# Kernel optimization log

Measured on AMD Instinct MI355X. Metric: run time of the kernel, lower is better.

## Reference

```python
import jax, jax.numpy as jnp
import numpy as np

B, T, C, HS = 8, 2048, 1024, 64

def setup_inputs() -> dict:
    key = jax.random.key(0)
    ks = jax.random.split(key, 6)
    return {
        "q_vec": jax.random.normal(ks[0], (B, T, C), dtype=jnp.float32),
        "k_vec": jax.random.normal(ks[1], (B, T, C), dtype=jnp.float32),
        "v_vec": jax.random.normal(ks[2], (B, T, C), dtype=jnp.float32),
        "mask": jnp.ones((B, T), dtype=jnp.int32),
        "Wq": jax.random.normal(ks[3], (C, HS), dtype=jnp.float32) * (C ** -0.5),
        "Wk": jax.random.normal(ks[4], (C, HS), dtype=jnp.float32) * (C ** -0.5),
        "Wv": jax.random.normal(ks[5], (C, HS), dtype=jnp.float32) * (C ** -0.5),
    }

def reference(q_vec, k_vec, v_vec, mask, Wq, Wk, Wv):
    # bias-free linear projections: [B,T,C] @ [C,HS] -> [B,T,HS]
    q = jnp.einsum('btc,ch->bth', q_vec, Wq)
    k = jnp.einsum('btc,ch->bth', k_vec, Wk)
    v = jnp.einsum('btc,ch->bth', v_vec, Wv)
    scale = k.shape[-1] ** -0.5
    # full T x T score matrix, as in the original module
    scores = jnp.einsum('bth,bsh->bts', q, k) * scale  # [B,T,T]
    Tq = scores.shape[1]
    # _expand_along_time: expanded[b,i,j] = mask[b,j], then causal tril
    mask_exp = jnp.broadcast_to(mask[:, None, :].astype(jnp.float32), scores.shape)
    tril = jnp.tril(jnp.ones((Tq, Tq), dtype=jnp.float32))
    combined = mask_exp * tril[None, :, :]
    scores = jnp.where(combined == 0, -jnp.inf, scores)
    attn = jax.nn.softmax(scores, axis=-1)
    # dropout p=0.0 (eval) -> identity
    out = jnp.einsum('bts,bsh->bth', attn, v)  # [B,T,HS]
    return out
```

## Files before the change

### kernel.cpp

```cpp
#include <hip/hip_runtime.h>
#include <hip/hip_bf16.h>
#include <cmath>
#include <stdint.h>

#define B_ 8
#define T_ 2048
#define C_ 1024
#define HS_ 64
#define NS 8
#define LP 72

typedef __attribute__((ext_vector_type(8))) short short8;
typedef __attribute__((ext_vector_type(4))) float floatx4;

__device__ inline unsigned short f2bf(float f) {
    union { float f; unsigned u; } v; v.f = f;
    unsigned r = v.u + 0x7FFF + ((v.u >> 16) & 1);
    return (unsigned short)(r >> 16);
}
__device__ inline unsigned pk2bf(float a, float b) {
    union { __hip_bfloat162 h; unsigned u; } v;
    v.h = __float22bfloat162_rn(float2{a, b});
    return v.u;
}
__device__ inline float bf2f(unsigned short u) {
    union { unsigned u; float f; } w; w.u = ((unsigned)u) << 16; return w.f;
}

__global__ __launch_bounds__(256) void prep_wt(const float* __restrict__ Wq,
                                               const float* __restrict__ Wk,
                                               const float* __restrict__ Wv,
                                               unsigned short* __restrict__ wt) {
    int p = blockIdx.x >> 4;
    int chunk = blockIdx.x & 15;
    const float* W = (p == 0) ? Wq : (p == 1) ? Wk : Wv;
    unsigned short* WT = wt + p * (C_ * HS_);
    int base = chunk * 4096;
    for (int i = threadIdx.x; i < 4096; i += 256) {
        int idx = base + i;
        int k = idx >> 6, n = idx & 63;
        WT[n * C_ + k] = f2bf(W[idx]);
    }
}

__global__ __launch_bounds__(256) void proj_kernel(
    const float* __restrict__ qv, const float* __restrict__ kv, const float* __restrict__ vv,
    const unsigned short* __restrict__ wt,
    unsigned short* __restrict__ qb, unsigned short* __restrict__ kb, unsigned short* __restrict__ vb)
{
    const int tid  = threadIdx.x;
    const int wave = tid >> 6, lane = tid & 63, quad = lane >> 4, l16 = lane & 15;
    const int wid  = blockIdx.x * 4 + wave;
    const int p    = wid >> 10;
    const int tile = wid & 1023;

    const float* X = (p == 0) ? qv : (p == 1) ? kv : vv;
    const unsigned short* WT = wt + p * (C_ * HS_);
    unsigned short* Ob = (p == 0) ? qb : (p == 1) ? kb : vb;
    const float oscale = (p == 0) ? 0.125f : 1.0f;

    const float* xp = X + ((long)tile * 16 + l16) * C_ + quad * 8;
    const unsigned short* wp = WT + l16 * C_ + quad * 8;

    floatx4 acc[4] = { {0,0,0,0},{0,0,0,0},{0,0,0,0},{0,0,0,0} };

    floatx4 xa, xb;
    short8 bfr0, bfr1, bfr2, bfr3;
    xa = *(const floatx4*)(xp);
    xb = *(const floatx4*)(xp + 4);
    bfr0 = *(const short8*)(wp + 0 * 16 * C_);
    bfr1 = *(const short8*)(wp + 1 * 16 * C_);
    bfr2 = *(const short8*)(wp + 2 * 16 * C_);
    bfr3 = *(const short8*)(wp + 3 * 16 * C_);

    #pragma unroll 4
    for (int ks = 0; ks < 32; ++ks) {
        floatx4 cx0 = xa, cx1 = xb;
        short8 cb0 = bfr0, cb1 = bfr1, cb2 = bfr2, cb3 = bfr3;
        if (ks + 1 < 32) {
            const int k0 = (ks + 1) * 32;
            xa = *(const floatx4*)(xp + k0);
            xb = *(const floatx4*)(xp + k0 + 4);
            bfr0 = *(const short8*)(wp + 0 * 16 * C_ + k0);
            bfr1 = *(const short8*)(wp + 1 * 16 * C_ + k0);
            bfr2 = *(const short8*)(wp + 2 * 16 * C_ + k0);
            bfr3 = *(const short8*)(wp + 3 * 16 * C_ + k0);
        }
        union { short8 s; unsigned u[4]; } af;
        af.u[0] = pk2bf(cx0[0], cx0[1]);
        af.u[1] = pk2bf(cx0[2], cx0[3]);
        af.u[2] = pk2bf(cx1[0], cx1[1]);
        af.u[3] = pk2bf(cx1[2], cx1[3]);
        acc[0] = __builtin_amdgcn_mfma_f32_16x16x32_bf16(af.s, cb0, acc[0], 0, 0, 0);
        acc[1] = __builtin_amdgcn_mfma_f32_16x16x32_bf16(af.s, cb1, acc[1], 0, 0, 0);
        acc[2] = __builtin_amdgcn_mfma_f32_16x16x32_bf16(af.s, cb2, acc[2], 0, 0, 0);
        acc[3] = __builtin_amdgcn_mfma_f32_16x16x32_bf16(af.s, cb3, acc[3], 0, 0, 0);
    }

    unsigned short* op = Ob + ((long)tile * 16 + quad * 4) * HS_ + l16;
    #pragma unroll
    for (int nt = 0; nt < 4; ++nt)
        #pragma unroll
        for (int r = 0; r < 4; ++r)
            op[r * HS_ + nt * 16] = f2bf(acc[nt][r] * oscale);
}

__global__ __launch_bounds__(256) void attn_partial(
    const unsigned short* __restrict__ qb, const unsigned short* __restrict__ kb,
    const unsigned short* __restrict__ vb, const int* __restrict__ mask,
    unsigned short* __restrict__ Opart, float* __restrict__ Mpart, float* __restrict__ Lpart)
{
    const int s  = blockIdx.x & (NS - 1);
    const int bq = blockIdx.x >> 3;
    const int qt = bq & 31;
    const int b  = bq >> 5;
    if (s > qt) return;

    __shared__ unsigned short Klds[64 * LP];
    __shared__ unsigned short Vt[64 * LP];
    __shared__ unsigned short Plds[4][16 * LP];

    const int tid = threadIdx.x;
    const int wave = tid >> 6, lane = tid & 63, quad = lane >> 4, l16 = lane & 15;

    const int qrow = qt * 64 + wave * 16 + l16;
    const unsigned short* qp = qb + ((long)(b * T_ + qrow)) * HS_;
    short8 aq0 = *(const short8*)&qp[0  + quad * 8];
    short8 aq1 = *(const short8*)&qp[32 + quad * 8];

    floatx4 acc_o[4] = { {0,0,0,0},{0,0,0,0},{0,0,0,0},{0,0,0,0} };
    float m_r[4] = { -INFINITY, -INFINITY, -INFINITY, -INFINITY };
    float l_r[4] = { 0.f, 0.f, 0.f, 0.f };

    const int rowg = qt * 64 + wave * 16 + quad * 4;

    const int skey = tid >> 3;
    const int sf8  = (tid & 7) * 8;
    const int vp = tid & 31, vg = tid >> 5;

    for (int c = s; c <= qt; c += NS) {
        const int kc = c * 64;
        #pragma unroll
        for (int it = 0; it < 2; ++it) {
            int key = it * 32 + skey;
            *(short8*)&Klds[key * LP + sf8] =
                *(const short8*)&kb[((long)(b * T_ + kc + key)) * HS_ + sf8];
        }
        {
            const unsigned short* v0p = &vb[((long)(b * T_ + kc + 2 * vp)) * HS_ + vg * 8];
            short8 v0 = *(const short8*)v0p;
            short8 v1 = *(const short8*)(v0p + HS_);
            #pragma unroll
            for (int j = 0; j < 8; ++j) {
                unsigned pr = (unsigned)(unsigned short)v0[j] |
                              ((unsigned)(unsigned short)v1[j] << 16);
                *(unsigned*)&Vt[(vg * 8 + j) * LP + 2 * vp] = pr;
            }
        }
        __syncthreads();

        floatx4 sv[4];
        #pragma unroll
        for (int kt = 0; kt < 4; ++kt) {
            floatx4 a = {0.f, 0.f, 0.f, 0.f};
            short8 bk0 = *(short8*)&Klds[(kt * 16 + l16) * LP + 0  + quad * 8];
            short8 bk1 = *(short8*)&Klds[(kt * 16 + l16) * LP + 32 + quad * 8];
            a = __builtin_amdgcn_mfma_f32_16x16x32_bf16(aq0, bk0, a, 0, 0, 0);
            a = __builtin_amdgcn_mfma_f32_16x16x32_bf16(aq1, bk1, a, 0, 0, 0);
            sv[kt] = a;
        }

        const bool lastc = (c == qt);
        #pragma unroll
        for (int kt = 0; kt < 4; ++kt) {
            int key = kc + kt * 16 + l16;
            int mk = mask[b * T_ + key];
            #pragma unroll
            for (int r = 0; r < 4; ++r) {
                bool dead = (mk == 0) || (lastc && key > rowg + r);
                if (dead) sv[kt][r] = -INFINITY;
            }
        }

        float alpha[4];
        #pragma unroll
        for (int r = 0; r < 4; ++r) {
            float mx = fmaxf(fmaxf(sv[0][r], sv[1][r]), fmaxf(sv[2][r], sv[3][r]));
            #pragma unroll
            for (int off = 1; off < 16; off <<= 1)
                mx = fmaxf(mx, __shfl_xor(mx, off));
            float mn = fmaxf(m_r[r], mx);
            float a_ = __expf(m_r[r] - mn);
            float ps = 0.f;
            #pragma unroll
            for (int kt = 0; kt < 4; ++kt) {
                float pv = __expf(sv[kt][r] - mn);
                sv[kt][r] = pv;
                ps += pv;
            }
            #pragma unroll
            for (int off = 1; off < 16; off <<= 1)
                ps += __shfl_xor(ps, off);
            l_r[r] = l_r[r] * a_ + ps;
            m_r[r] = mn;
            alpha[r] = a_;
        }
        #pragma unroll
        for (int nt = 0; nt < 4; ++nt)
            #pragma unroll
            for (int r = 0; r < 4; ++r)
                acc_o[nt][r] *= alpha[r];

        unsigned short* pl = Plds[wave];
        #pragma unroll
        for (int kt = 0; kt < 4; ++kt)
            #pragma unroll
            for (int r = 0; r < 4; ++r)
                pl[(quad * 4 + r) * LP + kt * 16 + l16] = f2bf(sv[kt][r]);
        short8 ap0 = *(short8*)&pl[l16 * LP + 0  + quad * 8];
        short8 ap1 = *(short8*)&pl[l16 * LP + 32 + quad * 8];

        #pragma unroll
        for (int nt = 0; nt < 4; ++nt) {
            short8 bv0 = *(short8*)&Vt[(nt * 16 + l16) * LP + 0  + quad * 8];
            short8 bv1 = *(short8*)&Vt[(nt * 16 + l16) * LP + 32 + quad * 8];
            acc_o[nt] = __builtin_amdgcn_mfma_f32_16x16x32_bf16(ap0, bv0, acc_o[nt], 0, 0, 0);
            acc_o[nt] = __builtin_amdgcn_mfma_f32_16x16x32_bf16(ap1, bv1, acc_o[nt], 0, 0, 0);
        }
        __syncthreads();
    }

    unsigned short* Op = Opart + (long)blockIdx.x * 4096;
    #pragma unroll
    for (int nt = 0; nt < 4; ++nt)
        #pragma unroll
        for (int r = 0; r < 4; ++r)
            Op[(wave * 16 + quad * 4 + r) * 64 + nt * 16 + l16] = f2bf(acc_o[nt][r]);
    if (l16 == 0) {
        #pragma unroll
        for (int r = 0; r < 4; ++r) {
            int rl = wave * 16 + quad * 4 + r;
            Mpart[(long)blockIdx.x * 64 + rl] = m_r[r];
            Lpart[(long)blockIdx.x * 64 + rl] = l_r[r];
        }
    }
}

__global__ __launch_bounds__(256) void attn_combine(
    const unsigned short* __restrict__ Opart, const float* __restrict__ Mpart,
    const float* __restrict__ Lpart, float* __restrict__ out)
{
    const int half = blockIdx.x & 1;
    const int bq = blockIdx.x >> 1;
    const int qt = bq & 31;
    const int b  = bq >> 5;
    const int nsp = (qt + 1 < NS) ? qt + 1 : NS;

    const int row  = (threadIdx.x >> 3) + half * 32;
    const int colg = (threadIdx.x & 7) * 8;
    const long base = (long)bq * NS;

    float M = -INFINITY;
    #pragma unroll
    for (int sp = 0; sp < NS; ++sp)
        if (sp < nsp) M = fmaxf(M, Mpart[(base + sp) * 64 + row]);

    float w[NS];
    float L = 0.f;
    #pragma unroll
    for (int sp = 0; sp < NS; ++sp)
        if (sp < nsp) {
            float e = __expf(Mpart[(base + sp) * 64 + row] - M);
            w[sp] = e;
            L += e * Lpart[(base + sp) * 64 + row];
        }

    float acc[8] = {0,0,0,0,0,0,0,0};
    #pragma unroll
    for (int sp = 0; sp < NS; ++sp)
        if (sp < nsp) {
            const unsigned short* Op = Opart + (base + sp) * 4096 + row * 64 + colg;
            short8 o = *(const short8*)Op;
            float ws = w[sp];
            #pragma unroll
            for (int j = 0; j < 8; ++j)
                acc[j] += ws * bf2f((unsigned short)o[j]);
        }

    float inv = 1.0f / L;
    float* op = out + ((long)(b * T_ + qt * 64 + row)) * HS_ + colg;
    floatx4 o0 = { acc[0] * inv, acc[1] * inv, acc[2] * inv, acc[3] * inv };
    floatx4 o1 = { acc[4] * inv, acc[5] * inv, acc[6] * inv, acc[7] * inv };
    *(floatx4*)op = o0;
    *(floatx4*)(op + 4) = o1;
}

extern "C" void kernel_launch(void* const* d_in, const int* in_sizes, int n_in,
                              void* d_out, int out_size, void* d_ws, size_t ws_size,
                              hipStream_t stream)
{
    const float* qv = (const float*)d_in[0];
    const float* kv = (const float*)d_in[1];
    const float* vv = (const float*)d_in[2];
    const int*   mask = (const int*)d_in[3];
    const float* Wq = (const float*)d_in[4];
    const float* Wk = (const float*)d_in[5];
    const float* Wv = (const float*)d_in[6];
    float* out = (float*)d_out;

    unsigned short* wt    = (unsigned short*)d_ws;
    unsigned short* qbuf  = wt + 3 * C_ * HS_;
    unsigned short* kbuf  = qbuf + (long)B_ * T_ * HS_;
    unsigned short* vbuf  = kbuf + (long)B_ * T_ * HS_;
    unsigned short* Opart = vbuf + (long)B_ * T_ * HS_;
    float* Mpart = (float*)(Opart + (long)B_ * 32 * NS * 4096);
    float* Lpart = Mpart + (long)B_ * 32 * NS * 64;

    prep_wt<<<48, 256, 0, stream>>>(Wq, Wk, Wv, wt);
    proj_kernel<<<768, 256, 0, stream>>>(qv, kv, vv, wt, qbuf, kbuf, vbuf);
    attn_partial<<<B_ * 32 * NS, 256, 0, stream>>>(qbuf, kbuf, vbuf, mask, Opart, Mpart, Lpart);
    attn_combine<<<B_ * 32 * 2, 256, 0, stream>>>(Opart, Mpart, Lpart, out);
}
```

Baseline: 276.3 us.

## Stage projection weights in LDS and share across four waves per block

```diff
diff --git a/kernel.cpp b/kernel.cpp
--- a/kernel.cpp
+++ b/kernel.cpp
@@ -9,6 +9,7 @@
 #define HS_ 64
 #define NS 8
 #define LP 72
+#define PLP 520
 
 typedef __attribute__((ext_vector_type(8))) short short8;
 typedef __attribute__((ext_vector_type(4))) float floatx4;
@@ -48,56 +49,96 @@
     const unsigned short* __restrict__ wt,
     unsigned short* __restrict__ qb, unsigned short* __restrict__ kb, unsigned short* __restrict__ vb)
 {
+    __shared__ unsigned short Wl[64 * PLP];
+
     const int tid  = threadIdx.x;
     const int wave = tid >> 6, lane = tid & 63, quad = lane >> 4, l16 = lane & 15;
-    const int wid  = blockIdx.x * 4 + wave;
-    const int p    = wid >> 10;
-    const int tile = wid & 1023;
+    const int bid  = blockIdx.x;
+    const int p    = bid >> 8;
+    const int t64  = bid & 255;
 
     const float* X = (p == 0) ? qv : (p == 1) ? kv : vv;
     const unsigned short* WT = wt + p * (C_ * HS_);
     unsigned short* Ob = (p == 0) ? qb : (p == 1) ? kb : vb;
     const float oscale = (p == 0) ? 0.125f : 1.0f;
 
-    const float* xp = X + ((long)tile * 16 + l16) * C_ + quad * 8;
-    const unsigned short* wp = WT + l16 * C_ + quad * 8;
+    const int srow = (tid >> 6) * 4 + 0;
+    short8 wreg[16];
+    #pragma unroll
+    for (int it = 0; it < 16; ++it) {
+        int u = it * 256 + tid;
+        int row = u >> 6, c16 = u & 63;
+        wreg[it] = *(const short8*)(WT + row * C_ + c16 * 8);
+    }
+    #pragma unroll
+    for (int it = 0; it < 16; ++it) {
+        int u = it * 256 + tid;
+        int row = u >> 6, c16 = u & 63;
+        *(short8*)&Wl[row * PLP + c16 * 8] = wreg[it];
+    }
+    __syncthreads();
+    (void)srow;
+
+    short8 wreg2[16];
+    #pragma unroll
+    for (int it = 0; it < 16; ++it) {
+        int u = it * 256 + tid;
+        int row = u >> 6, c16 = u & 63;
+        wreg2[it] = *(const short8*)(WT + row * C_ + 512 + c16 * 8);
+    }
+
+    const float* xp = X + ((long)t64 * 64 + wave * 16 + l16) * C_ + quad * 8;
 
     floatx4 acc[4] = { {0,0,0,0},{0,0,0,0},{0,0,0,0},{0,0,0,0} };
 
-    floatx4 xa, xb;
-    short8 bfr0, bfr1, bfr2, bfr3;
-    xa = *(const floatx4*)(xp);
-    xb = *(const floatx4*)(xp + 4);
-    bfr0 = *(const short8*)(wp + 0 * 16 * C_);
-    bfr1 = *(const short8*)(wp + 1 * 16 * C_);
-    bfr2 = *(const short8*)(wp + 2 * 16 * C_);
-    bfr3 = *(const short8*)(wp + 3 * 16 * C_);
-
-    #pragma unroll 4
-    for (int ks = 0; ks < 32; ++ks) {
-        floatx4 cx0 = xa, cx1 = xb;
-        short8 cb0 = bfr0, cb1 = bfr1, cb2 = bfr2, cb3 = bfr3;
-        if (ks + 1 < 32) {
-            const int k0 = (ks + 1) * 32;
-            xa = *(const floatx4*)(xp + k0);
-            xb = *(const floatx4*)(xp + k0 + 4);
-            bfr0 = *(const short8*)(wp + 0 * 16 * C_ + k0);
-            bfr1 = *(const short8*)(wp + 1 * 16 * C_ + k0);
-            bfr2 = *(const short8*)(wp + 2 * 16 * C_ + k0);
-            bfr3 = *(const short8*)(wp + 3 * 16 * C_ + k0);
-        }
-        union { short8 s; unsigned u[4]; } af;
-        af.u[0] = pk2bf(cx0[0], cx0[1]);
-        af.u[1] = pk2bf(cx0[2], cx0[3]);
-        af.u[2] = pk2bf(cx1[0], cx1[1]);
-        af.u[3] = pk2bf(cx1[2], cx1[3]);
-        acc[0] = __builtin_amdgcn_mfma_f32_16x16x32_bf16(af.s, cb0, acc[0], 0, 0, 0);
-        acc[1] = __builtin_amdgcn_mfma_f32_16x16x32_bf16(af.s, cb1, acc[1], 0, 0, 0);
-        acc[2] = __builtin_amdgcn_mfma_f32_16x16x32_bf16(af.s, cb2, acc[2], 0, 0, 0);
-        acc[3] = __builtin_amdgcn_mfma_f32_16x16x32_bf16(af.s, cb3, acc[3], 0, 0, 0);
-    }
-
-    unsigned short* op = Ob + ((long)tile * 16 + quad * 4) * HS_ + l16;
+    #pragma unroll
+    for (int h = 0; h < 2; ++h) {
+        const float* xh = xp + h * 512;
+        floatx4 x0a = *(const floatx4*)(xh + 0);
+        floatx4 x0b = *(const floatx4*)(xh + 4);
+        floatx4 x1a = *(const floatx4*)(xh + 32);
+        floatx4 x1b = *(const floatx4*)(xh + 36);
+
+        #pragma unroll
+        for (int ks = 0; ks < 16; ++ks) {
+            floatx4 ca, cb;
+            if (ks & 1) { ca = x1a; cb = x1b; } else { ca = x0a; cb = x0b; }
+            if (ks + 2 < 16) {
+                const float* nx = xh + (ks + 2) * 32;
+                if (ks & 1) { x1a = *(const floatx4*)nx; x1b = *(const floatx4*)(nx + 4); }
+                else        { x0a = *(const floatx4*)nx; x0b = *(const floatx4*)(nx + 4); }
+            }
+            union { short8 s; unsigned u[4]; } af;
+            af.u[0] = pk2bf(ca[0], ca[1]);
+            af.u[1] = pk2bf(ca[2], ca[3]);
+            af.u[2] = pk2bf(cb[0], cb[1]);
+            af.u[3] = pk2bf(cb[2], cb[3]);
+
+            const unsigned short* wl = &Wl[l16 * PLP + ks * 32 + quad * 8];
+            short8 b0 = *(const short8*)(wl + 0 * 16 * PLP);
+            short8 b1 = *(const short8*)(wl + 1 * 16 * PLP);
+            short8 b2 = *(const short8*)(wl + 2 * 16 * PLP);
+            short8 b3 = *(const short8*)(wl + 3 * 16 * PLP);
+
+            acc[0] = __builtin_amdgcn_mfma_f32_16x16x32_bf16(af.s, b0, acc[0], 0, 0, 0);
+            acc[1] = __builtin_amdgcn_mfma_f32_16x16x32_bf16(af.s, b1, acc[1], 0, 0, 0);
+            acc[2] = __builtin_amdgcn_mfma_f32_16x16x32_bf16(af.s, b2, acc[2], 0, 0, 0);
+            acc[3] = __builtin_amdgcn_mfma_f32_16x16x32_bf16(af.s, b3, acc[3], 0, 0, 0);
+        }
+
+        if (h == 0) {
+            __syncthreads();
+            #pragma unroll
+            for (int it = 0; it < 16; ++it) {
+                int u = it * 256 + tid;
+                int row = u >> 6, c16 = u & 63;
+                *(short8*)&Wl[row * PLP + c16 * 8] = wreg2[it];
+            }
+            __syncthreads();
+        }
+    }
+
+    unsigned short* op = Ob + ((long)t64 * 64 + wave * 16 + quad * 4) * HS_ + l16;
     #pragma unroll
     for (int nt = 0; nt < 4; ++nt)
         #pragma unroll
```

Result: faster. 260.8 us (-5.6%).
